# Kernel optimization log

Measured on AMD Instinct MI355X. Metric: run time of the kernel, lower is better.

## Reference

```python
import jax, jax.numpy as jnp
import numpy as np

N = 100_000      # nodes
E = 3_200_000    # edges (avg degree 32)
F_IN = 37        # NCI1 num_features
H = 16           # hidden
C = 2            # NCI1 num_classes


def setup_inputs() -> dict:
    key = jax.random.key(0)
    k = jax.random.split(key, 7)
    x = jax.random.normal(k[0], (N, F_IN), dtype=jnp.float32)
    edge_index = jax.random.randint(k[1], (2, E), 0, N, dtype=jnp.int32)
    edge_weight = jax.random.uniform(k[2], (E,), dtype=jnp.float32)
    # Glorot-ish init for the two GCN linear weights, zero bias (PyG default)
    W1 = jax.random.normal(k[3], (F_IN, H), dtype=jnp.float32) * (1.0 / np.sqrt(F_IN))
    b1 = jnp.zeros((H,), dtype=jnp.float32)
    W2 = jax.random.normal(k[4], (H, C), dtype=jnp.float32) * (1.0 / np.sqrt(H))
    b2 = jnp.zeros((C,), dtype=jnp.float32)
    return {"x": x, "edge_index": edge_index, "edge_weight": edge_weight,
            "W1": W1, "b1": b1, "W2": W2, "b2": b2}


def _gcn_norm(edge_index, edge_weight, dtype):
    # PyG gcn_norm: add self-loops (weight 1.0), symmetric D^-1/2 A D^-1/2
    loop = jnp.arange(N, dtype=edge_index.dtype)
    row = jnp.concatenate([edge_index[0], loop])  # source
    col = jnp.concatenate([edge_index[1], loop])  # target (aggregation index)
    w = jnp.concatenate([edge_weight, jnp.ones((N,), dtype=dtype)])
    deg = jax.ops.segment_sum(w, col, num_segments=N)
    dinv = jnp.where(deg > 0, jax.lax.rsqrt(deg), 0.0).astype(dtype)
    norm = dinv[row] * w * dinv[col]  # [E+N]
    return row, col, norm


def _gcn_layer(x, row, col, norm, W, b):
    h = x @ W                                   # small dense transform first
    msg = norm[:, None] * h[row]                # gather + scale, [E+N, out]
    out = jax.ops.segment_sum(msg, col, num_segments=N)  # scatter-add
    return out + b


def reference(x, edge_index, edge_weight, W1, b1, W2, b2):
    row, col, norm = _gcn_norm(edge_index, edge_weight, x.dtype)
    h = jax.nn.relu(_gcn_layer(x, row, col, norm, W1, b1))
    # F.dropout with training=False is identity (module evaluated in eval mode)
    h = _gcn_layer(h, row, col, norm, W2, b2)
    return jax.nn.log_softmax(h, axis=1)
```

## Files before the change

### kernel.cpp

```cpp
#include <hip/hip_runtime.h>
#include <math.h>

#define N_NODES 100000
#define N_EDGES 3200000
#define F_IN    37
#define H_DIM   16
#define C_DIM   2

#define BUCKET_BITS 7
#define BUCKET_SZ   128
#define NBUCK       782
#define CAP         4736
#define CHUNK       16384
#define NCHUNK      196
#define EPT         16
#define EPT_S       5

__device__ __forceinline__ unsigned bf16rne(float f) {
    unsigned u = __float_as_uint(f);
    return (u + 0x7FFFu + ((u >> 16) & 1u)) >> 16;
}
__device__ __forceinline__ int2 ldnt_i2(const int2* p) {
    long long v = __builtin_nontemporal_load((const long long*)p);
    return *(int2*)&v;
}
#define BLO(u) __uint_as_float((u) << 16)
#define BHI(u) __uint_as_float((u) & 0xFFFF0000u)
#define EW(u)  __uint_as_float(((u) >> 17) << 16)
#define ER(u)  ((u) & 0x1FFFFu)

__global__ void k_init(int* __restrict__ gcur) {
    int i = blockIdx.x * blockDim.x + threadIdx.x;
    if (i < NBUCK) gcur[i] = i * CAP;
}

__global__ __launch_bounds__(1024) void k_part(
    const int* __restrict__ row, const int* __restrict__ col,
    const float* __restrict__ w, int* __restrict__ gcur, int2* __restrict__ ebuf)
{
    __shared__ int cnt[NBUCK];
    __shared__ int gbase[NBUCK];
    int t = threadIdx.x;
    int e0 = blockIdx.x * CHUNK;
    int bk[EPT], rc[EPT], lofs[EPT];
    float wv[EPT];

    if (t < NBUCK) cnt[t] = 0;
    __syncthreads();
#pragma unroll
    for (int k = 0; k < EPT; k++) {
        int e = e0 + k * 1024 + t;
        if (e < N_EDGES) {
            int r = __builtin_nontemporal_load(&row[e]);
            int c = __builtin_nontemporal_load(&col[e]);
            wv[k] = __builtin_nontemporal_load(&w[e]);
            bk[k] = c >> BUCKET_BITS;
            rc[k] = r | ((c & (BUCKET_SZ - 1)) << 17);
            lofs[k] = atomicAdd(&cnt[bk[k]], 1);
        } else bk[k] = -1;
    }
    __syncthreads();
    if (t < NBUCK) gbase[t] = atomicAdd(&gcur[t], cnt[t]);
    __syncthreads();
#pragma unroll
    for (int k = 0; k < EPT; k++) {
        if (bk[k] >= 0)
            ebuf[gbase[bk[k]] + lofs[k]] = make_int2(rc[k], __float_as_int(wv[k]));
    }
}

__global__ __launch_bounds__(1024) void k_sortxw1(
    const int* __restrict__ gcur, const int2* __restrict__ ebuf,
    const float* __restrict__ x, const float* __restrict__ W1,
    unsigned* __restrict__ ebuf4, int2* __restrict__ rp,
    float* __restrict__ dinv, unsigned* __restrict__ h1b)
{
    __shared__ int2  stage[CAP];
    __shared__ int   cnt[BUCKET_SZ];
    __shared__ int   base[BUCKET_SZ];
    __shared__ float sdinv[BUCKET_SZ];
    __shared__ float sW[F_IN * H_DIM];
    float* xs = (float*)stage;

    int t = threadIdx.x, b = blockIdx.x;
    int s = b * CAP;
    int len = gcur[b] - s;
    int nbase = b << BUCKET_BITS;
    if (t < BUCKET_SZ) cnt[t] = 0;
    __syncthreads();

    int2 ed[EPT_S]; int cl[EPT_S], lofs[EPT_S];
#pragma unroll
    for (int k = 0; k < EPT_S; k++) {
        int i = k * 1024 + t;
        if (i < len) {
            int2 v = ldnt_i2(&ebuf[s + i]);
            ed[k] = v;
            cl[k] = v.x >> 17;
            lofs[k] = atomicAdd(&cnt[cl[k]], 1);
        } else cl[k] = -1;
    }
    __syncthreads();
    if (t < BUCKET_SZ) base[t] = cnt[t];
    __syncthreads();
    for (int off = 1; off < BUCKET_SZ; off <<= 1) {
        int v2 = 0;
        if (t < BUCKET_SZ && t >= off) v2 = base[t - off];
        __syncthreads();
        if (t < BUCKET_SZ) base[t] += v2;
        __syncthreads();
    }
#pragma unroll
    for (int k = 0; k < EPT_S; k++) {
        if (cl[k] >= 0) {
            int pos = base[cl[k]] - cnt[cl[k]] + lofs[k];
            stage[pos] = ed[k];
        }
    }
    __syncthreads();
    for (int i = t; i < len; i += 1024) {
        int2 v = stage[i];
        unsigned wb = bf16rne(__int_as_float(v.y));
        __builtin_nontemporal_store((wb << 17) | (unsigned)(v.x & 0x1FFFF),
                                    &ebuf4[s + i]);
    }
    if (t < BUCKET_SZ) {
        int c = nbase + t;
        int st = base[t] - cnt[t], n = cnt[t];
        float sum = 1.0f;
        for (int i = 0; i < n; i++) sum += __int_as_float(stage[st + i].y);
        float di = rsqrtf(sum);
        sdinv[t] = di;
        if (c < N_NODES) {
            rp[c] = make_int2(s + st, n);
            dinv[c] = di;
        }
    }
    __syncthreads();

    for (int idx = t; idx < F_IN * H_DIM; idx += 1024) sW[idx] = W1[idx];
    int g0 = nbase * F_IN;
    int nfl = BUCKET_SZ * F_IN;
    for (int idx = t; idx < nfl; idx += 1024) {
        int gi = g0 + idx;
        xs[idx] = (gi < N_NODES * F_IN) ? __builtin_nontemporal_load(&x[gi]) : 0.f;
    }
    __syncthreads();
    {
        int n = t >> 3, sub = t & 7;
        int c = nbase + n;
        if (c < N_NODES) {
            const float* xi = &xs[n * F_IN];
            float a0 = 0.f, a1 = 0.f;
            for (int k = 0; k < F_IN; k++) {
                float xv = xi[k];
                a0 += xv * sW[k * H_DIM + 2 * sub];
                a1 += xv * sW[k * H_DIM + 2 * sub + 1];
            }
            float di = sdinv[n];
            unsigned pk = bf16rne(di * a0) | (bf16rne(di * a1) << 16);
            h1b[(size_t)c * 8 + sub] = pk;
        }
    }
}

__global__ __launch_bounds__(256) void k_agg1(
    const int2* __restrict__ rp, const unsigned* __restrict__ ebuf4,
    const uint2* __restrict__ h1b, const float* __restrict__ dinv,
    const float* __restrict__ b1, const float* __restrict__ W2,
    float* __restrict__ h2s)
{
    __shared__ float sW2[H_DIM * C_DIM];
    __shared__ float sb1[H_DIM];
    int t = threadIdx.x;
    if (t < H_DIM * C_DIM) sW2[t] = W2[t];
    if (t >= 32 && t < 32 + H_DIM) sb1[t - 32] = b1[t - 32];
    __syncthreads();
    int id = blockIdx.x * 256 + t;
    int c = id >> 3;
    int sub = id & 7, q = sub & 3, h = sub >> 2;
    if (c >= N_NODES) return;
    int2 seg = rp[c];
    int s = seg.x, n = seg.y;
    int m = (n - h + 1) >> 1;
    int p0i = s + h;
    float4 acc = make_float4(0.f, 0.f, 0.f, 0.f);

#define PROC1(u)                                                    \
    {   float a = EW(u);                                            \
        uint2 g = h1b[(size_t)ER(u) * 4 + q];                       \
        acc.x += a * BLO(g.x); acc.y += a * BHI(g.x);               \
        acc.z += a * BLO(g.y); acc.w += a * BHI(g.y); }

    int k = 0;
    if (m >= 4) {
        unsigned e0 = __builtin_nontemporal_load(&ebuf4[p0i + 0]);
        unsigned e1 = __builtin_nontemporal_load(&ebuf4[p0i + 2]);
        unsigned e2 = __builtin_nontemporal_load(&ebuf4[p0i + 4]);
        unsigned e3 = __builtin_nontemporal_load(&ebuf4[p0i + 6]);
        for (; k + 8 <= m; k += 4) {
            unsigned f0 = __builtin_nontemporal_load(&ebuf4[p0i + 2 * (k + 4)]);
            unsigned f1 = __builtin_nontemporal_load(&ebuf4[p0i + 2 * (k + 5)]);
            unsigned f2 = __builtin_nontemporal_load(&ebuf4[p0i + 2 * (k + 6)]);
            unsigned f3 = __builtin_nontemporal_load(&ebuf4[p0i + 2 * (k + 7)]);
            PROC1(e0); PROC1(e1); PROC1(e2); PROC1(e3);
            e0 = f0; e1 = f1; e2 = f2; e3 = f3;
        }
        PROC1(e0); PROC1(e1); PROC1(e2); PROC1(e3);
        k += 4;
    }
    for (; k < m; k++) {
        unsigned u = __builtin_nontemporal_load(&ebuf4[p0i + 2 * k]);
        PROC1(u);
    }
#undef PROC1

    acc.x += __shfl_xor(acc.x, 4);
    acc.y += __shfl_xor(acc.y, 4);
    acc.z += __shfl_xor(acc.z, 4);
    acc.w += __shfl_xor(acc.w, 4);

    float dc = dinv[c];
    uint2 gc = h1b[(size_t)c * 4 + q];
    float hcv[4] = {BLO(gc.x), BHI(gc.x), BLO(gc.y), BHI(gc.y)};
    float av[4] = {acc.x + hcv[0], acc.y + hcv[1], acc.z + hcv[2], acc.w + hcv[3]};
    int j0 = q << 2;
    float p0 = 0.f, p1 = 0.f;
#pragma unroll
    for (int j = 0; j < 4; j++) {
        float rv = fmaxf(dc * av[j] + sb1[j0 + j], 0.f);
        p0 += rv * sW2[(j0 + j) * C_DIM + 0];
        p1 += rv * sW2[(j0 + j) * C_DIM + 1];
    }
    p0 += __shfl_xor(p0, 1); p0 += __shfl_xor(p0, 2);
    p1 += __shfl_xor(p1, 1); p1 += __shfl_xor(p1, 2);
    if (sub == 0) ((float2*)h2s)[c] = make_float2(dc * p0, dc * p1);
}

__global__ __launch_bounds__(256) void k_agg2(
    const int2* __restrict__ rp, const unsigned* __restrict__ ebuf4,
    const float* __restrict__ h2s, const float* __restrict__ dinv,
    const float* __restrict__ b2, float* __restrict__ out)
{
    int id = blockIdx.x * 256 + threadIdx.x;
    int c = id >> 2, sub = id & 3;
    if (c >= N_NODES) return;
    int2 seg = rp[c];
    int s = seg.x, n = seg.y;
    const float2* h22 = (const float2*)h2s;
    int m = (n - sub + 3) >> 2;
    int p0i = s + sub;
    float a0 = 0.f, a1 = 0.f;

#define PROC2(u)                                                    \
    {   float a = EW(u);                                            \
        float2 hv = h22[ER(u)];                                     \
        a0 += a * hv.x;  a1 += a * hv.y; }

    int k = 0;
    if (m >= 4) {
        unsigned e0 = __builtin_nontemporal_load(&ebuf4[p0i + 0]);
        unsigned e1 = __builtin_nontemporal_load(&ebuf4[p0i + 4]);
        unsigned e2 = __builtin_nontemporal_load(&ebuf4[p0i + 8]);
        unsigned e3 = __builtin_nontemporal_load(&ebuf4[p0i + 12]);
        for (; k + 8 <= m; k += 4) {
            unsigned f0 = __builtin_nontemporal_load(&ebuf4[p0i + 4 * (k + 4)]);
            unsigned f1 = __builtin_nontemporal_load(&ebuf4[p0i + 4 * (k + 5)]);
            unsigned f2 = __builtin_nontemporal_load(&ebuf4[p0i + 4 * (k + 6)]);
            unsigned f3 = __builtin_nontemporal_load(&ebuf4[p0i + 4 * (k + 7)]);
            PROC2(e0); PROC2(e1); PROC2(e2); PROC2(e3);
            e0 = f0; e1 = f1; e2 = f2; e3 = f3;
        }
        PROC2(e0); PROC2(e1); PROC2(e2); PROC2(e3);
        k += 4;
    }
    for (; k < m; k++) {
        unsigned u = __builtin_nontemporal_load(&ebuf4[p0i + 4 * k]);
        PROC2(u);
    }
#undef PROC2

    a0 += __shfl_xor(a0, 1); a0 += __shfl_xor(a0, 2);
    a1 += __shfl_xor(a1, 1); a1 += __shfl_xor(a1, 2);
    if (sub == 0) {
        float dc = dinv[c];
        float2 hc = h22[c];
        float l0 = dc * (a0 + hc.x) + b2[0];
        float l1 = dc * (a1 + hc.y) + b2[1];
        float mx = fmaxf(l0, l1);
        float lse = mx + logf(expf(l0 - mx) + expf(l1 - mx));
        ((float2*)out)[c] = make_float2(l0 - lse, l1 - lse);
    }
}

extern "C" void kernel_launch(void* const* d_in, const int* in_sizes, int n_in,
                              void* d_out, int out_size, void* d_ws, size_t ws_size,
                              hipStream_t stream) {
    const float* x  = (const float*)d_in[0];
    const int*   ei = (const int*)d_in[1];
    const float* w  = (const float*)d_in[2];
    const float* W1 = (const float*)d_in[3];
    const float* b1 = (const float*)d_in[4];
    const float* W2 = (const float*)d_in[5];
    const float* b2 = (const float*)d_in[6];
    float* out = (float*)d_out;

    const int* row = ei;
    const int* col = ei + N_EDGES;

    char* ws = (char*)d_ws;
    int*      gcur  = (int*)(ws + 0);
    int2*     rp    = (int2*)(ws + 3200);
    float*    dinv  = (float*)(ws + 803200);
    unsigned* h1b   = (unsigned*)(ws + 1203200);
    float*    h2s   = (float*)(ws + 4403200);
    unsigned* ebuf4 = (unsigned*)(ws + 5203200);
    int2*     ebuf  = (int2*)(ws + 20017408);

    k_init    <<<4, 256, 0, stream>>>(gcur);
    k_part    <<<NCHUNK, 1024, 0, stream>>>(row, col, w, gcur, ebuf);
    k_sortxw1 <<<NBUCK, 1024, 0, stream>>>(gcur, ebuf, x, W1, ebuf4, rp, dinv, h1b);
    k_agg1    <<<(8 * N_NODES + 255) / 256, 256, 0, stream>>>(rp, ebuf4, (const uint2*)h1b, dinv, b1, W2, h2s);
    k_agg2    <<<(4 * N_NODES + 255) / 256, 256, 0, stream>>>(rp, ebuf4, h2s, dinv, b2, out);
}
```

Baseline: 210.2 us.

## Widen per-node thread groups in aggregation and parallelize degree sums

The aggregation kernels now give each node twice as many threads: 16 lanes in layer 1 (4 edge phases times 4 feature quads) and 8 lanes in layer 2, with an extra shuffle stage to reduce. The degree sum in the sort kernel now uses 8 lanes per node with a shuffle reduction, replacing a serial loop over 128 threads. The init kernel becomes a memset, and the bucket base offset is added in the partition kernel. More threads per node aim to hide gather latency and shorten serial loops, at the cost of more idle lanes for low-degree nodes and extra shuffles.

After: 200.0 us. -4.8%, faster.

```diff
diff --git a/kernel.cpp b/kernel.cpp
--- a/kernel.cpp
+++ b/kernel.cpp
@@ -28,11 +28,6 @@
 #define BHI(u) __uint_as_float((u) & 0xFFFF0000u)
 #define EW(u)  __uint_as_float(((u) >> 17) << 16)
 #define ER(u)  ((u) & 0x1FFFFu)
-
-__global__ void k_init(int* __restrict__ gcur) {
-    int i = blockIdx.x * blockDim.x + threadIdx.x;
-    if (i < NBUCK) gcur[i] = i * CAP;
-}
 
 __global__ __launch_bounds__(1024) void k_part(
     const int* __restrict__ row, const int* __restrict__ col,
@@ -60,7 +55,7 @@
         } else bk[k] = -1;
     }
     __syncthreads();
-    if (t < NBUCK) gbase[t] = atomicAdd(&gcur[t], cnt[t]);
+    if (t < NBUCK) gbase[t] = t * CAP + atomicAdd(&gcur[t], cnt[t]);
     __syncthreads();
 #pragma unroll
     for (int k = 0; k < EPT; k++) {
@@ -84,7 +79,7 @@
 
     int t = threadIdx.x, b = blockIdx.x;
     int s = b * CAP;
-    int len = gcur[b] - s;
+    int len = gcur[b];
     int nbase = b << BUCKET_BITS;
     if (t < BUCKET_SZ) cnt[t] = 0;
     __syncthreads();
@@ -124,16 +119,22 @@
         __builtin_nontemporal_store((wb << 17) | (unsigned)(v.x & 0x1FFFF),
                                     &ebuf4[s + i]);
     }
-    if (t < BUCKET_SZ) {
-        int c = nbase + t;
-        int st = base[t] - cnt[t], n = cnt[t];
-        float sum = 1.0f;
-        for (int i = 0; i < n; i++) sum += __int_as_float(stage[st + i].y);
-        float di = rsqrtf(sum);
-        sdinv[t] = di;
-        if (c < N_NODES) {
-            rp[c] = make_int2(s + st, n);
-            dinv[c] = di;
+    {
+        int n = t >> 3, l = t & 7;
+        int st = base[n] - cnt[n], cn = cnt[n];
+        float sum = 0.f;
+        for (int i = l; i < cn; i += 8) sum += __int_as_float(stage[st + i].y);
+        sum += __shfl_xor(sum, 1);
+        sum += __shfl_xor(sum, 2);
+        sum += __shfl_xor(sum, 4);
+        if (l == 0) {
+            float di = rsqrtf(sum + 1.0f);
+            sdinv[n] = di;
+            int c = nbase + n;
+            if (c < N_NODES) {
+                rp[c] = make_int2(s + st, cn);
+                dinv[c] = di;
+            }
         }
     }
     __syncthreads();
@@ -177,12 +178,12 @@
     if (t >= 32 && t < 32 + H_DIM) sb1[t - 32] = b1[t - 32];
     __syncthreads();
     int id = blockIdx.x * 256 + t;
-    int c = id >> 3;
-    int sub = id & 7, q = sub & 3, h = sub >> 2;
+    int c = id >> 4;
+    int sub = id & 15, q = sub & 3, h = sub >> 2;
     if (c >= N_NODES) return;
     int2 seg = rp[c];
     int s = seg.x, n = seg.y;
-    int m = (n - h + 1) >> 1;
+    int m = (n - h + 3) >> 2;
     int p0i = s + h;
     float4 acc = make_float4(0.f, 0.f, 0.f, 0.f);
 
@@ -191,71 +192,6 @@
         uint2 g = h1b[(size_t)ER(u) * 4 + q];                       \
         acc.x += a * BLO(g.x); acc.y += a * BHI(g.x);               \
         acc.z += a * BLO(g.y); acc.w += a * BHI(g.y); }
-
-    int k = 0;
-    if (m >= 4) {
-        unsigned e0 = __builtin_nontemporal_load(&ebuf4[p0i + 0]);
-        unsigned e1 = __builtin_nontemporal_load(&ebuf4[p0i + 2]);
-        unsigned e2 = __builtin_nontemporal_load(&ebuf4[p0i + 4]);
-        unsigned e3 = __builtin_nontemporal_load(&ebuf4[p0i + 6]);
-        for (; k + 8 <= m; k += 4) {
-            unsigned f0 = __builtin_nontemporal_load(&ebuf4[p0i + 2 * (k + 4)]);
-            unsigned f1 = __builtin_nontemporal_load(&ebuf4[p0i + 2 * (k + 5)]);
-            unsigned f2 = __builtin_nontemporal_load(&ebuf4[p0i + 2 * (k + 6)]);
-            unsigned f3 = __builtin_nontemporal_load(&ebuf4[p0i + 2 * (k + 7)]);
-            PROC1(e0); PROC1(e1); PROC1(e2); PROC1(e3);
-            e0 = f0; e1 = f1; e2 = f2; e3 = f3;
-        }
-        PROC1(e0); PROC1(e1); PROC1(e2); PROC1(e3);
-        k += 4;
-    }
-    for (; k < m; k++) {
-        unsigned u = __builtin_nontemporal_load(&ebuf4[p0i + 2 * k]);
-        PROC1(u);
-    }
-#undef PROC1
-
-    acc.x += __shfl_xor(acc.x, 4);
-    acc.y += __shfl_xor(acc.y, 4);
-    acc.z += __shfl_xor(acc.z, 4);
-    acc.w += __shfl_xor(acc.w, 4);
-
-    float dc = dinv[c];
-    uint2 gc = h1b[(size_t)c * 4 + q];
-    float hcv[4] = {BLO(gc.x), BHI(gc.x), BLO(gc.y), BHI(gc.y)};
-    float av[4] = {acc.x + hcv[0], acc.y + hcv[1], acc.z + hcv[2], acc.w + hcv[3]};
-    int j0 = q << 2;
-    float p0 = 0.f, p1 = 0.f;
-#pragma unroll
-    for (int j = 0; j < 4; j++) {
-        float rv = fmaxf(dc * av[j] + sb1[j0 + j], 0.f);
-        p0 += rv * sW2[(j0 + j) * C_DIM + 0];
-        p1 += rv * sW2[(j0 + j) * C_DIM + 1];
-    }
-    p0 += __shfl_xor(p0, 1); p0 += __shfl_xor(p0, 2);
-    p1 += __shfl_xor(p1, 1); p1 += __shfl_xor(p1, 2);
-    if (sub == 0) ((float2*)h2s)[c] = make_float2(dc * p0, dc * p1);
-}
-
-__global__ __launch_bounds__(256) void k_agg2(
-    const int2* __restrict__ rp, const unsigned* __restrict__ ebuf4,
-    const float* __restrict__ h2s, const float* __restrict__ dinv,
-    const float* __restrict__ b2, float* __restrict__ out)
-{
-    int id = blockIdx.x * 256 + threadIdx.x;
-    int c = id >> 2, sub = id & 3;
-    if (c >= N_NODES) return;
-    int2 seg = rp[c];
-    int s = seg.x, n = seg.y;
-    const float2* h22 = (const float2*)h2s;
-    int m = (n - sub + 3) >> 2;
-    int p0i = s + sub;
-    float a0 = 0.f, a1 = 0.f;
-
-#define PROC2(u)                                                    \
-    {   float a = EW(u);                                            \
-        float2 hv = h22[ER(u)];                                     \
-        a0 += a * hv.x;  a1 += a * hv.y; }
 
     int k = 0;
     if (m >= 4) {
@@ -268,6 +204,71 @@
             unsigned f1 = __builtin_nontemporal_load(&ebuf4[p0i + 4 * (k + 5)]);
             unsigned f2 = __builtin_nontemporal_load(&ebuf4[p0i + 4 * (k + 6)]);
             unsigned f3 = __builtin_nontemporal_load(&ebuf4[p0i + 4 * (k + 7)]);
+            PROC1(e0); PROC1(e1); PROC1(e2); PROC1(e3);
+            e0 = f0; e1 = f1; e2 = f2; e3 = f3;
+        }
+        PROC1(e0); PROC1(e1); PROC1(e2); PROC1(e3);
+        k += 4;
+    }
+    for (; k < m; k++) {
+        unsigned u = __builtin_nontemporal_load(&ebuf4[p0i + 4 * k]);
+        PROC1(u);
+    }
+#undef PROC1
+
+    acc.x += __shfl_xor(acc.x, 4);  acc.x += __shfl_xor(acc.x, 8);
+    acc.y += __shfl_xor(acc.y, 4);  acc.y += __shfl_xor(acc.y, 8);
+    acc.z += __shfl_xor(acc.z, 4);  acc.z += __shfl_xor(acc.z, 8);
+    acc.w += __shfl_xor(acc.w, 4);  acc.w += __shfl_xor(acc.w, 8);
+
+    float dc = dinv[c];
+    uint2 gc = h1b[(size_t)c * 4 + q];
+    float hcv[4] = {BLO(gc.x), BHI(gc.x), BLO(gc.y), BHI(gc.y)};
+    float av[4] = {acc.x + hcv[0], acc.y + hcv[1], acc.z + hcv[2], acc.w + hcv[3]};
+    int j0 = q << 2;
+    float p0 = 0.f, p1 = 0.f;
+#pragma unroll
+    for (int j = 0; j < 4; j++) {
+        float rv = fmaxf(dc * av[j] + sb1[j0 + j], 0.f);
+        p0 += rv * sW2[(j0 + j) * C_DIM + 0];
+        p1 += rv * sW2[(j0 + j) * C_DIM + 1];
+    }
+    p0 += __shfl_xor(p0, 1); p0 += __shfl_xor(p0, 2);
+    p1 += __shfl_xor(p1, 1); p1 += __shfl_xor(p1, 2);
+    if (sub == 0) ((float2*)h2s)[c] = make_float2(dc * p0, dc * p1);
+}
+
+__global__ __launch_bounds__(256) void k_agg2(
+    const int2* __restrict__ rp, const unsigned* __restrict__ ebuf4,
+    const float* __restrict__ h2s, const float* __restrict__ dinv,
+    const float* __restrict__ b2, float* __restrict__ out)
+{
+    int id = blockIdx.x * 256 + threadIdx.x;
+    int c = id >> 3, sub = id & 7;
+    if (c >= N_NODES) return;
+    int2 seg = rp[c];
+    int s = seg.x, n = seg.y;
+    const float2* h22 = (const float2*)h2s;
+    int m = (n - sub + 7) >> 3;
+    int p0i = s + sub;
+    float a0 = 0.f, a1 = 0.f;
+
+#define PROC2(u)                                                    \
+    {   float a = EW(u);                                            \
+        float2 hv = h22[ER(u)];                                     \
+        a0 += a * hv.x;  a1 += a * hv.y; }
+
+    int k = 0;
+    if (m >= 4) {
+        unsigned e0 = __builtin_nontemporal_load(&ebuf4[p0i + 0]);
+        unsigned e1 = __builtin_nontemporal_load(&ebuf4[p0i + 8]);
+        unsigned e2 = __builtin_nontemporal_load(&ebuf4[p0i + 16]);
+        unsigned e3 = __builtin_nontemporal_load(&ebuf4[p0i + 24]);
+        for (; k + 8 <= m; k += 4) {
+            unsigned f0 = __builtin_nontemporal_load(&ebuf4[p0i + 8 * (k + 4)]);
+            unsigned f1 = __builtin_nontemporal_load(&ebuf4[p0i + 8 * (k + 5)]);
+            unsigned f2 = __builtin_nontemporal_load(&ebuf4[p0i + 8 * (k + 6)]);
+            unsigned f3 = __builtin_nontemporal_load(&ebuf4[p0i + 8 * (k + 7)]);
             PROC2(e0); PROC2(e1); PROC2(e2); PROC2(e3);
             e0 = f0; e1 = f1; e2 = f2; e3 = f3;
         }
@@ -275,13 +276,13 @@
         k += 4;
     }
     for (; k < m; k++) {
-        unsigned u = __builtin_nontemporal_load(&ebuf4[p0i + 4 * k]);
+        unsigned u = __builtin_nontemporal_load(&ebuf4[p0i + 8 * k]);
         PROC2(u);
     }
 #undef PROC2
 
-    a0 += __shfl_xor(a0, 1); a0 += __shfl_xor(a0, 2);
-    a1 += __shfl_xor(a1, 1); a1 += __shfl_xor(a1, 2);
+    a0 += __shfl_xor(a0, 1); a0 += __shfl_xor(a0, 2); a0 += __shfl_xor(a0, 4);
+    a1 += __shfl_xor(a1, 1); a1 += __shfl_xor(a1, 2); a1 += __shfl_xor(a1, 4);
     if (sub == 0) {
         float dc = dinv[c];
         float2 hc = h22[c];
@@ -317,9 +318,9 @@
     unsigned* ebuf4 = (unsigned*)(ws + 5203200);
     int2*     ebuf  = (int2*)(ws + 20017408);
 
-    k_init    <<<4, 256, 0, stream>>>(gcur);
+    hipMemsetAsync(gcur, 0, 3200, stream);
     k_part    <<<NCHUNK, 1024, 0, stream>>>(row, col, w, gcur, ebuf);
     k_sortxw1 <<<NBUCK, 1024, 0, stream>>>(gcur, ebuf, x, W1, ebuf4, rp, dinv, h1b);
-    k_agg1    <<<(8 * N_NODES + 255) / 256, 256, 0, stream>>>(rp, ebuf4, (const uint2*)h1b, dinv, b1, W2, h2s);
-    k_agg2    <<<(4 * N_NODES + 255) / 256, 256, 0, stream>>>(rp, ebuf4, h2s, dinv, b2, out);
-}
+    k_agg1    <<<(16 * N_NODES + 255) / 256, 256, 0, stream>>>(rp, ebuf4, (const uint2*)h1b, dinv, b1, W2, h2s);
+    k_agg2    <<<(8 * N_NODES + 255) / 256, 256, 0, stream>>>(rp, ebuf4, h2s, dinv, b2, out);
+}
```
